# Optimization experiments

Hardware: AMD Instinct MI355X
Metric: run time of the kernel (lower is better)

Reference implementation:

```python
import jax, jax.numpy as jnp
import numpy as np

NUM_HEADS = 16
HEAD_DIM = 64  # latent_dim // num_heads = 1024 // 16


def setup_inputs() -> dict:
    key = jax.random.key(0)
    k1, k2, k3, k4 = jax.random.split(key, 4)
    B, S, C = 4, 2048, 1024
    x = jax.random.normal(k1, (B, S, C), dtype=jnp.float32)
    # torch nn.Linear weight layout: [out_features, in_features]
    W_qkv = jax.random.normal(k2, (2 * 1024 + C, C), dtype=jnp.float32) * (C ** -0.5)
    W_out = jax.random.normal(k3, (C, C), dtype=jnp.float32) * (C ** -0.5)
    b_out = jax.random.normal(k4, (C,), dtype=jnp.float32) * 0.01
    return {"x": x, "W_qkv": W_qkv, "W_out": W_out, "b_out": b_out}


def reference(x, W_qkv, W_out, b_out):
    B, S, C = x.shape
    H, CH = NUM_HEADS, HEAD_DIM
    qkv = jnp.einsum('bsc,oc->bso', x, W_qkv)          # [B, S, 2*latent + C]
    qkv = qkv.reshape(B, S, H, -1)                      # per-head: [CH, CH, C//H]
    q = qkv[..., :CH]
    k = qkv[..., CH:2 * CH]
    v = qkv[..., 2 * CH:]
    energy = jnp.einsum('bqhc,bkhc->bhqk', q, k)        # full score matrix
    scale = jnp.asarray(C, x.dtype) ** 0.5              # note: original scales by sqrt(C), not sqrt(head_dim)
    attn = jax.nn.softmax(energy / scale, axis=-1)
    out = jnp.einsum('bhqk,bkhc->bqhc', attn, v).reshape(B, S, -1)
    out = jnp.einsum('bsc,oc->bso', out, W_out) + b_out
    return out + x
```

## Files before the change

kernel.cpp:

```cpp
#include <hip/hip_runtime.h>
#include <hip/hip_bf16.h>
#include <stdint.h>

#define BB 4
#define SS 2048
#define CC 1024
#define HH 16
#define DD 64
#define MTOT (BB*SS)
#define NQKV 3072

typedef __attribute__((ext_vector_type(8))) short short8;
typedef __attribute__((ext_vector_type(4))) float f32x4;
typedef __attribute__((ext_vector_type(16))) float f32x16;
typedef __attribute__((ext_vector_type(4))) unsigned uint4v;

#define MFMA16(A,B,C) __builtin_amdgcn_mfma_f32_16x16x32_bf16((A),(B),(C),0,0,0)
#define MFMA32(A,B,C) __builtin_amdgcn_mfma_f32_32x32x16_bf16((A),(B),(C),0,0,0)
#define BARRIER() asm volatile("s_barrier" ::: "memory")

__device__ __forceinline__ ushort f2bf(float f) {
  uint32_t u = __builtin_bit_cast(uint32_t, f);
  u += 0x7FFFu + ((u >> 16) & 1u);
  return (ushort)(u >> 16);
}

__device__ __forceinline__ float bf2f(ushort u) {
  return __builtin_bit_cast(float, (uint32_t)u << 16);
}

__device__ __forceinline__ unsigned cvtpk(float lo, float hi) {
  unsigned r;
  asm("v_cvt_pk_bf16_f32 %0, %1, %2" : "=v"(r) : "v"(lo), "v"(hi));
  return r;
}

__device__ __forceinline__ float hw_exp2(float x) {
  float r;
  asm("v_exp_f32 %0, %1" : "=v"(r) : "v"(x));
  return r;
}

__device__ __forceinline__ f32x16 zero16() {
  f32x16 v;
  #pragma unroll
  for (int i = 0; i < 16; ++i) v[i] = 0.f;
  return v;
}

__global__ void cvt3_kernel(const float* __restrict__ a, ushort* __restrict__ da, int na4,
                            const float* __restrict__ b, ushort* __restrict__ db, int nb4,
                            const float* __restrict__ c, ushort* __restrict__ dc, int nc4) {
  int total = na4 + nb4 + nc4;
  int stride = gridDim.x * blockDim.x;
  for (int i = blockIdx.x * blockDim.x + threadIdx.x; i < total; i += stride) {
    const float4* s; ushort4* d; int k;
    if (i < na4)            { s = (const float4*)a; d = (ushort4*)da; k = i; }
    else if (i < na4 + nb4) { s = (const float4*)b; d = (ushort4*)db; k = i - na4; }
    else                    { s = (const float4*)c; d = (ushort4*)dc; k = i - na4 - nb4; }
    float4 v = s[k];
    ushort4 o;
    o.x = f2bf(v.x); o.y = f2bf(v.y); o.z = f2bf(v.z); o.w = f2bf(v.w);
    d[k] = o;
  }
}

__device__ __forceinline__ void stage_half128(const ushort* __restrict__ gsrc, ushort* ldsbase, int tid) {
  #pragma unroll
  for (int ld = 0; ld < 4; ++ld) {
    int ci = ld * 256 + tid;
    int row = ci >> 3, slot = ci & 7;
    const ushort* src = gsrc + (size_t)row * 1024 + ((slot ^ (row & 7)) << 3);
    __builtin_amdgcn_global_load_lds(
        (const __attribute__((address_space(1))) uint32_t*)src,
        (__attribute__((address_space(3))) uint32_t*)(ldsbase + ci * 8), 16, 0, 0);
  }
}

__device__ __forceinline__ short8 rd_frag(const ushort* Lb, int row, int slot) {
  return *(const short8*)(Lb + row * 64 + ((slot ^ (row & 7)) << 3));
}

__device__ __forceinline__ void core128(const ushort* __restrict__ A, const ushort* __restrict__ Bw,
                                        int m0, int n0, ushort* L, f32x4 acc[4][4]) {
  const int tid = threadIdx.x, lane = tid & 63, w = tid >> 6;
  const int q = lane & 15, g = lane >> 4;
  const int wm = (w >> 1) * 64, wn = (w & 1) * 64;
  const ushort* Ag = A + (size_t)m0 * 1024;
  const ushort* Bg = Bw + (size_t)n0 * 1024;

  #pragma unroll
  for (int tt = 0; tt < 2; ++tt) {
    stage_half128(Ag + tt * 64, L + tt * 16384, tid);
    stage_half128(Bg + tt * 64, L + tt * 16384 + 8192, tid);
  }
  asm volatile("s_waitcnt vmcnt(8)" ::: "memory");
  BARRIER();

  #pragma unroll 1
  for (int t = 0; t < 16; ++t) {
    const ushort* La = L + (t & 1) * 16384;
    const ushort* Lb = La + 8192;
    short8 af[4][2], bf[4][2];
    #pragma unroll
    for (int mi = 0; mi < 4; ++mi)
      #pragma unroll
      for (int ks = 0; ks < 2; ++ks)
        af[mi][ks] = rd_frag(La, wm + mi * 16 + q, ks * 4 + g);
    #pragma unroll
    for (int nj = 0; nj < 4; ++nj)
      #pragma unroll
      for (int ks = 0; ks < 2; ++ks)
        bf[nj][ks] = rd_frag(Lb, wn + nj * 16 + q, ks * 4 + g);
    #pragma unroll
    for (int mi = 0; mi < 4; ++mi)
      #pragma unroll
      for (int nj = 0; nj < 4; ++nj) {
        acc[mi][nj] = MFMA16(af[mi][0], bf[nj][0], acc[mi][nj]);
        acc[mi][nj] = MFMA16(af[mi][1], bf[nj][1], acc[mi][nj]);
      }
    BARRIER();
    if (t <= 13) {
      ushort* Ls = L + (t & 1) * 16384;
      stage_half128(Ag + (t + 2) * 64, Ls, tid);
      stage_half128(Bg + (t + 2) * 64, Ls + 8192, tid);
      asm volatile("s_waitcnt vmcnt(8)" ::: "memory");
      BARRIER();
    } else if (t == 14) {
      asm volatile("s_waitcnt vmcnt(0)" ::: "memory");
      BARRIER();
    }
  }
}

__global__ __launch_bounds__(256, 2) void gemm_qkv(const ushort* __restrict__ xb, const ushort* __restrict__ wqkv,
                                                   ushort* __restrict__ qfbuf, ushort* __restrict__ kfbuf,
                                                   ushort* __restrict__ vfbuf) {
  __shared__ __align__(16) ushort L[32768];
  const int bid = blockIdx.x;
  const int xcd = bid & 7, r0 = bid >> 3;
  const int m0 = (r0 / 3) * 128, n0 = (xcd * 3 + (r0 % 3)) * 128;

  f32x4 acc[4][4];
  #pragma unroll
  for (int i = 0; i < 4; ++i)
    #pragma unroll
    for (int j = 0; j < 4; ++j) acc[i][j] = f32x4{0.f, 0.f, 0.f, 0.f};
  core128(xb, wqkv, m0, n0, L, acc);

  const int lane = threadIdx.x & 63, wave = threadIdx.x >> 6;
  const int g = lane >> 4, q = lane & 15;
  const int wm = (wave >> 1) * 64, wn = (wave & 1) * 64;
  const int s0 = m0 & 2047, bb = m0 >> 11;

  #pragma unroll
  for (int j = 0; j < 4; ++j) {
    int n = n0 + wn + j * 16 + q;
    int h = n / 192;
    int which = (n - h * 192) >> 6;
    float scl = (which == 0) ? 0.045084222f : 1.0f;
    int nc = wn + j * 16 + q;
    #pragma unroll
    for (int i = 0; i < 4; ++i) {
      #pragma unroll
      for (int rr = 0; rr < 4; ++rr) {
        int mr = wm + i * 16 + g * 4 + rr;
        L[mr * 128 + (nc ^ ((mr & 7) << 4))] = f2bf(acc[i][j][rr] * scl);
      }
    }
  }
  __syncthreads();

  {
    const int n_g = n0 + wave * 32;
    const int h = n_g / 192, rem = n_g - h * 192, which = rem >> 6;
    const int bh = bb * 16 + h;
    if (which < 2) {
      ushort* dst0 = (which == 0) ? qfbuf : kfbuf;
      const int c0 = (rem & 63) >> 5;
      #pragma unroll
      for (int k = 0; k < 8; ++k) {
        int jt = (s0 >> 4) + k;
        int mr = k * 16 + (lane & 15);
        int nc0 = wave * 32 + (lane >> 4) * 8;
        short8 v = *(const short8*)(L + mr * 128 + (nc0 ^ ((mr & 7) << 4)));
        *(short8*)(dst0 + ((((size_t)bh * 128 + jt) * 2 + c0) * 64 + lane) * 8) = v;
      }
    } else {
      const int ct0 = (rem & 63) >> 4;
      #pragma unroll
      for (int k = 0; k < 8; ++k) {
        int jcr = k >> 1, ct = ct0 + (k & 1);
        int nc = wave * 32 + (k & 1) * 16 + (lane & 15);
        int mrb = jcr * 32 + (lane >> 4) * 8;
        short8 v;
        #pragma unroll
        for (int e = 0; e < 8; ++e) {
          int mr = mrb + e;
          v[e] = (short)L[mr * 128 + (nc ^ ((mr & 7) << 4))];
        }
        int jc = (s0 >> 5) + jcr;
        *(short8*)(vfbuf + ((((size_t)bh * 64 + jc) * 4 + ct) * 64 + lane) * 8) = v;
      }
    }
  }
}

__global__ __launch_bounds__(256, 2) void gemm_out(const ushort* __restrict__ ab, const ushort* __restrict__ wout,
                                                   const ushort* __restrict__ xbb, const float* __restrict__ bias,
                                                   float* __restrict__ out) {
  __shared__ __align__(16) ushort L[32768];
  const int bid = blockIdx.x;
  const int sw = (bid & 7) * 64 + (bid >> 3);
  const int m0 = (sw & 63) * 128, n0 = (sw >> 6) * 128;

  f32x4 acc[4][4];
  #pragma unroll
  for (int i = 0; i < 4; ++i)
    #pragma unroll
    for (int j = 0; j < 4; ++j) acc[i][j] = f32x4{0.f, 0.f, 0.f, 0.f};
  core128(ab, wout, m0, n0, L, acc);

  const int tid = threadIdx.x;
  const int lane = tid & 63, wave = tid >> 6;
  const int g = lane >> 4, q = lane & 15;
  const int wm = (wave >> 1) * 64, wn = (wave & 1) * 64;
  float* Lf = reinterpret_cast<float*>(L);

  #pragma unroll
  for (int j = 0; j < 4; ++j) {
    int nc = wn + j * 16 + q;
    #pragma unroll
    for (int i = 0; i < 4; ++i) {
      #pragma unroll
      for (int rr = 0; rr < 4; ++rr) {
        int mr = wm + i * 16 + g * 4 + rr;
        int swz = ((mr & 4) << 0) | ((mr & 8) << 1);
        Lf[mr * 128 + (nc ^ swz)] = acc[i][j][rr];
      }
    }
  }
  __syncthreads();

  #pragma unroll
  for (int k = 0; k < 16; ++k) {
    int ci = k * 256 + tid;
    int row = ci >> 5, cb = (ci & 31) * 4;
    int swz = ((row & 4) << 0) | ((row & 8) << 1);
    float4 v = *(const float4*)(Lf + row * 128 + (cb ^ swz));
    size_t m = (size_t)(m0 + row);
    int n = n0 + cb;
    ushort4 xr = *(const ushort4*)(xbb + m * 1024 + n);
    float4 bv = *(const float4*)(bias + n);
    float4 o;
    o.x = v.x + bv.x + bf2f(xr.x);
    o.y = v.y + bv.y + bf2f(xr.y);
    o.z = v.z + bv.z + bf2f(xr.z);
    o.w = v.w + bv.w + bf2f(xr.w);
    *(float4*)(out + m * 1024 + n) = o;
  }
}

__global__ __launch_bounds__(256) void attn_kernel(const ushort* __restrict__ QF, const ushort* __restrict__ KF,
                                                   const ushort* __restrict__ VF, ushort* __restrict__ aout) {
  const int bid = blockIdx.x;
  const int xcd = bid & 7, r = bid >> 3;
  const int qb = r & 15, bh = xcd + (r >> 4) * 8;
  const int lane = threadIdx.x & 63, wave = threadIdx.x >> 6;
  const int l31 = lane & 31, hi = lane >> 5, l15 = lane & 15, l31h = l31 >> 4;
  const int qt = qb * 4 + wave;

  const ushort* QFb = QF + (size_t)bh * 131072;
  const ushort* KFb = KF + (size_t)bh * 131072;
  const ushort* VFb = VF + (size_t)bh * 131072;

  short8 onesf;
  #pragma unroll
  for (int e = 0; e < 8; ++e) onesf[e] = (short)0x3F80;

  short8 qf[4];
  #pragma unroll
  for (int kc = 0; kc < 4; ++kc) {
    int jt16 = qt * 2 + l31h;
    int lane2 = (((kc * 2 + hi) & 3) << 4) + l15;
    qf[kc] = *(const short8*)(QFb + ((size_t)(jt16 * 2 + (kc >> 1)) * 64 + lane2) * 8);
  }

  f32x16 oa0 = zero16(), oa1 = zero16(), la = zero16();

  short8 kfA[4], kfB[4], vf[2][2];
  #pragma unroll
  for (int kc = 0; kc < 4; ++kc) {
    int lane2 = (((kc * 2 + hi) & 3) << 4) + l15;
    kfA[kc] = *(const short8*)(KFb + ((size_t)(l31h * 2 + (kc >> 1)) * 64 + lane2) * 8);
  }

  #pragma unroll 1
  for (int j0 = 0; j0 < SS; j0 += 32) {
    #pragma unroll
    for (int kj = 0; kj < 2; ++kj)
      #pragma unroll
      for (int cb = 0; cb < 2; ++cb) {
        int ct = cb * 2 + l31h;
        int lane16 = (((kj * 2 + hi) & 3) << 4) + l15;
        vf[kj][cb] = *(const short8*)(VFb + ((size_t)((j0 >> 5) * 4 + ct) * 64 + lane16) * 8);
      }
    if (j0 + 32 < SS) {
      #pragma unroll
      for (int kc = 0; kc < 4; ++kc) {
        int jt16 = ((j0 + 32) >> 4) + l31h;
        int lane2 = (((kc * 2 + hi) & 3) << 4) + l15;
        kfB[kc] = *(const short8*)(KFb + ((size_t)(jt16 * 2 + (kc >> 1)) * 64 + lane2) * 8);
      }
    }

    f32x16 sa = zero16();
    __builtin_amdgcn_s_setprio(1);
    #pragma unroll
    for (int kc = 0; kc < 4; ++kc) sa = MFMA32(kfA[kc], qf[kc], sa);
    __builtin_amdgcn_s_setprio(0);

    unsigned w[8];
    #pragma unroll
    for (int i = 0; i < 8; ++i)
      w[i] = cvtpk(hw_exp2(sa[2 * i]), hw_exp2(sa[2 * i + 1]));

    #pragma unroll
    for (int kj = 0; kj < 2; ++kj) {
      unsigned a0 = w[kj * 4 + 0], a1 = w[kj * 4 + 1];
      unsigned b0 = w[kj * 4 + 2], b1 = w[kj * 4 + 3];
      unsigned sa0 = __shfl_xor(a0, 32, 64), sa1 = __shfl_xor(a1, 32, 64);
      unsigned sb0 = __shfl_xor(b0, 32, 64), sb1 = __shfl_xor(b1, 32, 64);
      uint4v t;
      t.x = hi ? sb0 : a0;
      t.y = hi ? sb1 : a1;
      t.z = hi ? b0 : sa0;
      t.w = hi ? b1 : sa1;
      short8 pa = __builtin_bit_cast(short8, t);
      __builtin_amdgcn_s_setprio(1);
      oa0 = MFMA32(pa, vf[kj][0], oa0);
      oa1 = MFMA32(pa, vf[kj][1], oa1);
      la  = MFMA32(pa, onesf, la);
      __builtin_amdgcn_s_setprio(0);
    }

    #pragma unroll
    for (int kc = 0; kc < 4; ++kc) kfA[kc] = kfB[kc];
  }

  const int b = bh >> 4, h = bh & 15;
  #pragma unroll
  for (int r16 = 0; r16 < 16; ++r16) {
    float inv = 1.0f / la[r16];
    int row = qt * 32 + (r16 & 3) + 8 * (r16 >> 2) + 4 * hi;
    size_t base = ((size_t)b * SS + row) * CC + h * DD;
    aout[base + l31]      = f2bf(oa0[r16] * inv);
    aout[base + 32 + l31] = f2bf(oa1[r16] * inv);
  }
}

extern "C" void kernel_launch(void* const* d_in, const int* in_sizes, int n_in,
                              void* d_out, int out_size, void* d_ws, size_t ws_size,
                              hipStream_t stream) {
  const float* x    = (const float*)d_in[0];
  const float* wqkv = (const float*)d_in[1];
  const float* wout = (const float*)d_in[2];
  const float* bias = (const float*)d_in[3];
  float* out = (float*)d_out;

  ushort* xb    = (ushort*)d_ws;
  ushort* wqkvb = xb + (size_t)8 * 1024 * 1024;
  ushort* woutb = wqkvb + (size_t)3 * 1024 * 1024;
  ushort* qfbuf = woutb + (size_t)1024 * 1024;
  ushort* kfbuf = qfbuf + (size_t)8 * 1024 * 1024;
  ushort* vfbuf = kfbuf + (size_t)8 * 1024 * 1024;
  ushort* aout  = vfbuf + (size_t)8 * 1024 * 1024;

  hipLaunchKernelGGL(cvt3_kernel, dim3(2048), dim3(256), 0, stream,
                     x, xb, 8 * 1024 * 1024 / 4,
                     wqkv, wqkvb, 3 * 1024 * 1024 / 4,
                     wout, woutb, 1024 * 1024 / 4);

  hipLaunchKernelGGL(gemm_qkv, dim3(1536), dim3(256), 0, stream,
                     xb, wqkvb, qfbuf, kfbuf, vfbuf);
  hipLaunchKernelGGL(attn_kernel, dim3(1024), dim3(256), 0, stream,
                     qfbuf, kfbuf, vfbuf, aout);
  hipLaunchKernelGGL(gemm_out, dim3(512), dim3(256), 0, stream,
                     aout, woutb, xb, bias, out);
}
```

Before: 210.6 us.

## Unroll attention loop by two with ping-pong K/V registers and permlane32 swap

The attention inner loop now processes 64 keys per iteration as two 32-key steps, alternating between two K and two V register buffers so loads for the next step are issued before the current step's MFMAs. This removes the per-iteration kfA=kfB copy. The cross-half P transpose now uses v_permlane32_swap instead of four ds_swizzle/shfl_xor operations plus selects. The cost is more live VGPRs for the doubled V buffers, which may lower occupancy.

After: 200.2 us. 1.05x faster.

```diff
diff --git a/kernel.cpp b/kernel.cpp
--- a/kernel.cpp
+++ b/kernel.cpp
@@ -14,6 +14,7 @@
 typedef __attribute__((ext_vector_type(4))) float f32x4;
 typedef __attribute__((ext_vector_type(16))) float f32x16;
 typedef __attribute__((ext_vector_type(4))) unsigned uint4v;
+typedef __attribute__((ext_vector_type(2))) unsigned uint2v;
 
 #define MFMA16(A,B,C) __builtin_amdgcn_mfma_f32_16x16x32_bf16((A),(B),(C),0,0,0)
 #define MFMA32(A,B,C) __builtin_amdgcn_mfma_f32_32x32x16_bf16((A),(B),(C),0,0,0)
@@ -261,6 +262,38 @@
   }
 }
 
+__device__ __forceinline__ void attn_step32(const short8 kf[4], const short8 vf[2][2],
+                                            const short8 qf[4], const short8 onesf,
+                                            f32x16& oa0, f32x16& oa1, f32x16& la, int hi) {
+  f32x16 sa = zero16();
+  __builtin_amdgcn_s_setprio(1);
+  #pragma unroll
+  for (int kc = 0; kc < 4; ++kc) sa = MFMA32(kf[kc], qf[kc], sa);
+  __builtin_amdgcn_s_setprio(0);
+
+  unsigned w[8];
+  #pragma unroll
+  for (int i = 0; i < 8; ++i)
+    w[i] = cvtpk(hw_exp2(sa[2 * i]), hw_exp2(sa[2 * i + 1]));
+
+  #pragma unroll
+  for (int kj = 0; kj < 2; ++kj) {
+    uint2v p0 = __builtin_amdgcn_permlane32_swap(w[kj * 4 + 2], w[kj * 4 + 0], false, false);
+    uint2v p1 = __builtin_amdgcn_permlane32_swap(w[kj * 4 + 3], w[kj * 4 + 1], false, false);
+    uint4v t;
+    t.x = p0[1];
+    t.y = p1[1];
+    t.z = p0[0];
+    t.w = p1[0];
+    short8 pa = __builtin_bit_cast(short8, t);
+    __builtin_amdgcn_s_setprio(1);
+    oa0 = MFMA32(pa, vf[kj][0], oa0);
+    oa1 = MFMA32(pa, vf[kj][1], oa1);
+    la  = MFMA32(pa, onesf, la);
+    __builtin_amdgcn_s_setprio(0);
+  }
+}
+
 __global__ __launch_bounds__(256) void attn_kernel(const ushort* __restrict__ QF, const ushort* __restrict__ KF,
                                                    const ushort* __restrict__ VF, ushort* __restrict__ aout) {
   const int bid = blockIdx.x;
@@ -288,7 +321,7 @@
 
   f32x16 oa0 = zero16(), oa1 = zero16(), la = zero16();
 
-  short8 kfA[4], kfB[4], vf[2][2];
+  short8 kfA[4], kfB[4], vfA[2][2], vfB[2][2];
   #pragma unroll
   for (int kc = 0; kc < 4; ++kc) {
     int lane2 = (((kc * 2 + hi) & 3) << 4) + l15;
@@ -296,56 +329,42 @@
   }
 
   #pragma unroll 1
-  for (int j0 = 0; j0 < SS; j0 += 32) {
+  for (int j0 = 0; j0 < SS; j0 += 64) {
     #pragma unroll
     for (int kj = 0; kj < 2; ++kj)
       #pragma unroll
       for (int cb = 0; cb < 2; ++cb) {
         int ct = cb * 2 + l31h;
         int lane16 = (((kj * 2 + hi) & 3) << 4) + l15;
-        vf[kj][cb] = *(const short8*)(VFb + ((size_t)((j0 >> 5) * 4 + ct) * 64 + lane16) * 8);
-      }
-    if (j0 + 32 < SS) {
+        vfA[kj][cb] = *(const short8*)(VFb + ((size_t)((j0 >> 5) * 4 + ct) * 64 + lane16) * 8);
+      }
+    #pragma unroll
+    for (int kc = 0; kc < 4; ++kc) {
+      int jt16 = ((j0 + 32) >> 4) + l31h;
+      int lane2 = (((kc * 2 + hi) & 3) << 4) + l15;
+      kfB[kc] = *(const short8*)(KFb + ((size_t)(jt16 * 2 + (kc >> 1)) * 64 + lane2) * 8);
+    }
+
+    attn_step32(kfA, vfA, qf, onesf, oa0, oa1, la, hi);
+
+    #pragma unroll
+    for (int kj = 0; kj < 2; ++kj)
+      #pragma unroll
+      for (int cb = 0; cb < 2; ++cb) {
+        int ct = cb * 2 + l31h;
+        int lane16 = (((kj * 2 + hi) & 3) << 4) + l15;
+        vfB[kj][cb] = *(const short8*)(VFb + ((size_t)(((j0 + 32) >> 5) * 4 + ct) * 64 + lane16) * 8);
+      }
+    if (j0 + 64 < SS) {
       #pragma unroll
       for (int kc = 0; kc < 4; ++kc) {
-        int jt16 = ((j0 + 32) >> 4) + l31h;
+        int jt16 = ((j0 + 64) >> 4) + l31h;
         int lane2 = (((kc * 2 + hi) & 3) << 4) + l15;
-        kfB[kc] = *(const short8*)(KFb + ((size_t)(jt16 * 2 + (kc >> 1)) * 64 + lane2) * 8);
-      }
-    }
-
-    f32x16 sa = zero16();
-    __builtin_amdgcn_s_setprio(1);
-    #pragma unroll
-    for (int kc = 0; kc < 4; ++kc) sa = MFMA32(kfA[kc], qf[kc], sa);
-    __builtin_amdgcn_s_setprio(0);
-
-    unsigned w[8];
-    #pragma unroll
-    for (int i = 0; i < 8; ++i)
-      w[i] = cvtpk(hw_exp2(sa[2 * i]), hw_exp2(sa[2 * i + 1]));
-
-    #pragma unroll
-    for (int kj = 0; kj < 2; ++kj) {
-      unsigned a0 = w[kj * 4 + 0], a1 = w[kj * 4 + 1];
-      unsigned b0 = w[kj * 4 + 2], b1 = w[kj * 4 + 3];
-      unsigned sa0 = __shfl_xor(a0, 32, 64), sa1 = __shfl_xor(a1, 32, 64);
-      unsigned sb0 = __shfl_xor(b0, 32, 64), sb1 = __shfl_xor(b1, 32, 64);
-      uint4v t;
-      t.x = hi ? sb0 : a0;
-      t.y = hi ? sb1 : a1;
-      t.z = hi ? b0 : sa0;
-      t.w = hi ? b1 : sa1;
-      short8 pa = __builtin_bit_cast(short8, t);
-      __builtin_amdgcn_s_setprio(1);
-      oa0 = MFMA32(pa, vf[kj][0], oa0);
-      oa1 = MFMA32(pa, vf[kj][1], oa1);
-      la  = MFMA32(pa, onesf, la);
-      __builtin_amdgcn_s_setprio(0);
-    }
-
-    #pragma unroll
-    for (int kc = 0; kc < 4; ++kc) kfA[kc] = kfB[kc];
+        kfA[kc] = *(const short8*)(KFb + ((size_t)(jt16 * 2 + (kc >> 1)) * 64 + lane2) * 8);
+      }
+    }
+
+    attn_step32(kfB, vfB, qf, onesf, oa0, oa1, la, hi);
   }
 
   const int b = bh >> 4, h = bh & 15;
```
